# Kernel tuning notes

Hardware: AMD Instinct MI355X
Metric: run time of the kernel (lower is better)

Reference implementation:

```python
import jax, jax.numpy as jnp
import numpy as np

KERNEL = (3, 3, 3, 3)
PAD = (1, 1, 1, 1)
IN_CH = 8
OUT_CH = 8


def setup_inputs() -> dict:
    key = jax.random.key(0)
    k1, k2, k3 = jax.random.split(key, 3)
    x = jax.random.normal(k1, (2, IN_CH, 7, 7, 48, 48), dtype=jnp.float32)
    K = KERNEL[0] * KERNEL[1] * KERNEL[2] * KERNEL[3]
    conv = jax.random.normal(k2, (OUT_CH, K * IN_CH), dtype=jnp.float32) * 0.05
    bias = jax.random.normal(k3, (OUT_CH,), dtype=jnp.float32) * 0.05
    return {"x": x, "conv": conv, "bias": bias}


def reference(x, conv, bias):
    # x: (B, C, u, v, h, w); conv: (oc, k0*k1*k2*k3*C); bias: (oc,)
    B, C, u, v, h, w = x.shape
    oc = conv.shape[0]
    k0, k1, k2, k3 = KERNEL
    # torch unfold+permute orders the contraction axis as (k0,k1,k2,k3,C)
    W = conv.reshape(oc, k0, k1, k2, k3, C)
    xp = jnp.pad(x, ((0, 0), (0, 0),
                     (PAD[0], PAD[0]), (PAD[1], PAD[1]),
                     (PAD[2], PAD[2]), (PAD[3], PAD[3])))
    out = jnp.zeros((B, oc, u, v, h, w), dtype=x.dtype)
    # stride = 1 everywhere: accumulate over the 3^4 kernel offsets
    for i0 in range(k0):
        for i1 in range(k1):
            for i2 in range(k2):
                for i3 in range(k3):
                    xs = xp[:, :, i0:i0 + u, i1:i1 + v, i2:i2 + h, i3:i3 + w]
                    out = out + jnp.einsum('bcuvhw,oc->bouvhw', xs,
                                           W[:, i0, i1, i2, i3, :])
    out = out + bias[None, :, None, None, None, None]
    return out
```

## Files before the change

### kernel.cpp

```cpp
#include <hip/hip_runtime.h>


typedef __attribute__((ext_vector_type(8))) short short8;
typedef __attribute__((ext_vector_type(4))) float f32x4;
typedef __attribute__((ext_vector_type(2))) int   i32x2;

#define CSTRIDE (49 * 2304)
#define WP_OFF  3920000
#define WT_OFF  3940992

__device__ __forceinline__ unsigned short f2bf(float f) {
    union { float f; unsigned u; } v; v.f = f;
    unsigned u = v.u;
    return (unsigned short)((u + 0x7FFF + ((u >> 16) & 1)) >> 16);
}

__global__ __launch_bounds__(256)
void prep(const float* __restrict__ x, const float* __restrict__ conv,
          unsigned short* __restrict__ ws16) {
    int g = blockIdx.x * 256 + threadIdx.x;
    if (g < 245000) {
        unsigned short vals[8];
#pragma unroll
        for (int c = 0; c < 8; ++c) vals[c] = 0;
        int b  = g / 122500;
        int r  = g - b * 122500;
        int uv = r / 2500;
        int p  = r - uv * 2500;
        int hh = p / 50, ww = p - hh * 50;
        int h = hh - 1, w = ww - 1;
        if (((unsigned)h < 48u) && ((unsigned)w < 48u)) {
            const float* xb = x + ((size_t)b * 8 * 49 + uv) * 2304 + h * 48 + w;
#pragma unroll
            for (int c = 0; c < 8; ++c) vals[c] = f2bf(xb[(size_t)c * CSTRIDE]);
        }
        *(short8*)(ws16 + (size_t)g * 8) = *(const short8*)vals;
        return;
    }
    g -= 245000;
    if (g < 10496) {
        int tap = g >> 7;
        int r   = g & 127;
        int m   = r >> 3, j = r & 7;
        unsigned short v = 0;
        if (tap < 81 && m < 8) v = f2bf(conv[m * 648 + tap * 8 + j]);
        ws16[WP_OFF / 2 + g] = v;
        return;
    }
    g -= 10496;
    if (g < 8624) {
        int img  = g / 88, slot = g - img * 88;
        int b    = img / 49, uv = img - b * 49;
        int u    = uv / 7,   v  = uv - u * 7;
        int cu = 3 - (u == 0) - (u == 6);
        int cv = 3 - (v == 0) - (v == 6);
        int tab, wof;
        if (slot < cu * cv * 9) {
            int g9  = slot / 9, hw9 = slot - 9 * g9;
            int gi0 = g9 / cv,  gi1 = g9 - cv * gi0;
            int i0 = (u == 0) + gi0, i1 = (v == 0) + gi1;
            int uu = u + i0 - 1,     vv = v + i1 - 1;
            int i2 = hw9 / 3,        i3 = hw9 - 3 * i2;
            tab = (((b * 7 + uu) * 7 + vv) * 2500 + i2 * 50 + i3) * 16;
            wof = ((i0 * 3 + i1) * 9 + hw9) * 256;
        } else {
            tab = 0;
            wof = 81 * 256;
        }
        i32x2 e; e.x = tab; e.y = wof;
        *(i32x2*)((char*)ws16 + WT_OFF + (size_t)g * 8) = e;
    }
}

__global__ __launch_bounds__(128, 6)
void conv4d_mfma(const unsigned short* __restrict__ ws16,
                 const float* __restrict__ bias,
                 float* __restrict__ out) {
    const int img = blockIdx.y;
    const int b   = img / 49;
    const int uvr = img - b * 49;
    const int u   = uvr / 7;
    const int v   = uvr - u * 7;
    const int cu  = 3 - (u == 0) - (u == 6);
    const int cv  = 3 - (v == 0) - (v == 6);
    const int nchunk = (cu * cv * 9 + 3) >> 2;

    const int lane  = threadIdx.x & 63;
    const int wave  = threadIdx.x >> 6;
    const int n     = lane & 15;
    const int quad  = lane >> 4;
    const int sbase = blockIdx.x * 64 + wave * 32;

    int myoff0, myoff1;
    {
        int s0 = sbase + n;
        int h0 = s0 / 48, w0 = s0 - h0 * 48;
        myoff0 = (h0 * 50 + w0) * 16;
        int s1 = sbase + 16 + n;
        int h1 = s1 / 48, w1 = s1 - h1 * 48;
        myoff1 = (h1 * 50 + w1) * 16;
    }

    const char* base0 = (const char*)ws16;
    const char* wpb   = base0 + WP_OFF;
    const i32x2* tbl  = (const i32x2*)(base0 + WT_OFF) + img * 88;
    const int n16     = n * 16;

    i32x2 tw = tbl[quad];
    short8 wf  = *(const short8*)(wpb + tw.y + n16);
    short8 xf0 = *(const short8*)(base0 + tw.x + myoff0);
    short8 xf1 = *(const short8*)(base0 + tw.x + myoff1);

    f32x4 acc0 = (f32x4){0.f, 0.f, 0.f, 0.f};
    f32x4 acc1 = acc0;

    for (int c = 0; c < nchunk; ++c) {
        i32x2 twn = tbl[4 * (c + 1) + quad];
        short8 wfn  = *(const short8*)(wpb + twn.y + n16);
        short8 xf0n = *(const short8*)(base0 + twn.x + myoff0);
        short8 xf1n = *(const short8*)(base0 + twn.x + myoff1);
        acc0 = __builtin_amdgcn_mfma_f32_16x16x32_bf16(wf, xf0, acc0, 0, 0, 0);
        acc1 = __builtin_amdgcn_mfma_f32_16x16x32_bf16(wf, xf1, acc1, 0, 0, 0);
        wf = wfn; xf0 = xf0n; xf1 = xf1n;
    }

    if (quad < 2) {
        f32x4 bb = *(const f32x4*)(bias + quad * 4);
        float* ob = out + ((size_t)b * 8 * 49 + uvr) * 2304 + sbase + n;
#pragma unroll
        for (int r = 0; r < 4; ++r) {
            int o = quad * 4 + r;
            ob[(size_t)o * CSTRIDE]      = acc0[r] + bb[r];
            ob[(size_t)o * CSTRIDE + 16] = acc1[r] + bb[r];
        }
    }
}

extern "C" void kernel_launch(void* const* d_in, const int* in_sizes, int n_in,
                              void* d_out, int out_size, void* d_ws, size_t ws_size,
                              hipStream_t stream) {
    const float* x    = (const float*)d_in[0];
    const float* conv = (const float*)d_in[1];
    const float* bias = (const float*)d_in[2];
    float* out = (float*)d_out;
    unsigned short* ws16 = (unsigned short*)d_ws;

    prep<<<dim3((245000 + 10496 + 8624 + 255) / 256), dim3(256), 0, stream>>>(x, conv, ws16);
    conv4d_mfma<<<dim3(36, 98), dim3(128), 0, stream>>>(ws16, bias, out);
}
```

Before: 82.31 us.

## Pack tap table into single ints and fully unroll chunk loop with preloaded table

Each tap-table entry is packed into one 32-bit int holding the activation offset and weight-tap index, and a dedicated zero region replaces the padding entries. The conv kernel preloads all 21 table entries into registers up front and fully unrolls the MFMA chunk loop in three tiers (9, 14, 21 chunks) matching the possible boundary counts. This lets all gathers be issued early, removing the serial dependency on table loads in the software pipeline. The cost is more registers, so launch bounds are relaxed from 6 to 4 waves per SIMD, which may lower occupancy.

Result: faster. 78.59 us (-4.5%).

```diff
diff --git a/kernel.cpp b/kernel.cpp
--- a/kernel.cpp
+++ b/kernel.cpp
@@ -3,11 +3,11 @@
 
 typedef __attribute__((ext_vector_type(8))) short short8;
 typedef __attribute__((ext_vector_type(4))) float f32x4;
-typedef __attribute__((ext_vector_type(2))) int   i32x2;
 
 #define CSTRIDE (49 * 2304)
-#define WP_OFF  3920000
-#define WT_OFF  3940992
+#define ZS_OFF  3920000
+#define WP_OFF  3960000
+#define WT_OFF  3981504
 
 __device__ __forceinline__ unsigned short f2bf(float f) {
     union { float f; unsigned u; } v; v.f = f;
@@ -19,26 +19,28 @@
 void prep(const float* __restrict__ x, const float* __restrict__ conv,
           unsigned short* __restrict__ ws16) {
     int g = blockIdx.x * 256 + threadIdx.x;
-    if (g < 245000) {
+    if (g < 247500) {
         unsigned short vals[8];
 #pragma unroll
         for (int c = 0; c < 8; ++c) vals[c] = 0;
-        int b  = g / 122500;
-        int r  = g - b * 122500;
-        int uv = r / 2500;
-        int p  = r - uv * 2500;
-        int hh = p / 50, ww = p - hh * 50;
-        int h = hh - 1, w = ww - 1;
-        if (((unsigned)h < 48u) && ((unsigned)w < 48u)) {
-            const float* xb = x + ((size_t)b * 8 * 49 + uv) * 2304 + h * 48 + w;
+        if (g < 245000) {
+            int b  = g / 122500;
+            int r  = g - b * 122500;
+            int uv = r / 2500;
+            int p  = r - uv * 2500;
+            int hh = p / 50, ww = p - hh * 50;
+            int h = hh - 1, w = ww - 1;
+            if (((unsigned)h < 48u) && ((unsigned)w < 48u)) {
+                const float* xb = x + ((size_t)b * 8 * 49 + uv) * 2304 + h * 48 + w;
 #pragma unroll
-            for (int c = 0; c < 8; ++c) vals[c] = f2bf(xb[(size_t)c * CSTRIDE]);
+                for (int c = 0; c < 8; ++c) vals[c] = f2bf(xb[(size_t)c * CSTRIDE]);
+            }
         }
         *(short8*)(ws16 + (size_t)g * 8) = *(const short8*)vals;
         return;
     }
-    g -= 245000;
-    if (g < 10496) {
+    g -= 247500;
+    if (g < 10752) {
         int tap = g >> 7;
         int r   = g & 127;
         int m   = r >> 3, j = r & 7;
@@ -47,32 +49,31 @@
         ws16[WP_OFF / 2 + g] = v;
         return;
     }
-    g -= 10496;
+    g -= 10752;
     if (g < 8624) {
         int img  = g / 88, slot = g - img * 88;
         int b    = img / 49, uv = img - b * 49;
         int u    = uv / 7,   v  = uv - u * 7;
         int cu = 3 - (u == 0) - (u == 6);
         int cv = 3 - (v == 0) - (v == 6);
-        int tab, wof;
+        int entry;
         if (slot < cu * cv * 9) {
             int g9  = slot / 9, hw9 = slot - 9 * g9;
             int gi0 = g9 / cv,  gi1 = g9 - cv * gi0;
             int i0 = (u == 0) + gi0, i1 = (v == 0) + gi1;
             int uu = u + i0 - 1,     vv = v + i1 - 1;
             int i2 = hw9 / 3,        i3 = hw9 - 3 * i2;
-            tab = (((b * 7 + uu) * 7 + vv) * 2500 + i2 * 50 + i3) * 16;
-            wof = ((i0 * 3 + i1) * 9 + hw9) * 256;
+            int tab  = (((b * 7 + uu) * 7 + vv) * 2500 + i2 * 50 + i3) * 16;
+            int wtap = (i0 * 3 + i1) * 9 + hw9;
+            entry = tab | (wtap << 22);
         } else {
-            tab = 0;
-            wof = 81 * 256;
+            entry = ZS_OFF | (81 << 22);
         }
-        i32x2 e; e.x = tab; e.y = wof;
-        *(i32x2*)((char*)ws16 + WT_OFF + (size_t)g * 8) = e;
+        ((int*)((char*)ws16 + WT_OFF))[g] = entry;
     }
 }
 
-__global__ __launch_bounds__(128, 6)
+__global__ __launch_bounds__(128, 4)
 void conv4d_mfma(const unsigned short* __restrict__ ws16,
                  const float* __restrict__ bias,
                  float* __restrict__ out) {
@@ -103,26 +104,39 @@
 
     const char* base0 = (const char*)ws16;
     const char* wpb   = base0 + WP_OFF;
-    const i32x2* tbl  = (const i32x2*)(base0 + WT_OFF) + img * 88;
-    const int n16     = n * 16;
+    const int*  tblp  = (const int*)(base0 + WT_OFF) + img * 88;
+    const int   n16   = n * 16;
 
-    i32x2 tw = tbl[quad];
-    short8 wf  = *(const short8*)(wpb + tw.y + n16);
-    short8 xf0 = *(const short8*)(base0 + tw.x + myoff0);
-    short8 xf1 = *(const short8*)(base0 + tw.x + myoff1);
+    int t[21];
+#pragma unroll
+    for (int c = 0; c < 21; ++c) t[c] = tblp[4 * c + quad];
 
     f32x4 acc0 = (f32x4){0.f, 0.f, 0.f, 0.f};
     f32x4 acc1 = acc0;
 
-    for (int c = 0; c < nchunk; ++c) {
-        i32x2 twn = tbl[4 * (c + 1) + quad];
-        short8 wfn  = *(const short8*)(wpb + twn.y + n16);
-        short8 xf0n = *(const short8*)(base0 + twn.x + myoff0);
-        short8 xf1n = *(const short8*)(base0 + twn.x + myoff1);
-        acc0 = __builtin_amdgcn_mfma_f32_16x16x32_bf16(wf, xf0, acc0, 0, 0, 0);
-        acc1 = __builtin_amdgcn_mfma_f32_16x16x32_bf16(wf, xf1, acc1, 0, 0, 0);
-        wf = wfn; xf0 = xf0n; xf1 = xf1n;
+#define CHUNK(c)                                                              \
+    {                                                                         \
+        int e   = t[c];                                                       \
+        int tab = e & 0x3FFFFF;                                               \
+        int wof = (e >> 22) << 8;                                             \
+        short8 wf  = *(const short8*)(wpb + wof + n16);                       \
+        short8 xf0 = *(const short8*)(base0 + tab + myoff0);                  \
+        short8 xf1 = *(const short8*)(base0 + tab + myoff1);                  \
+        acc0 = __builtin_amdgcn_mfma_f32_16x16x32_bf16(wf, xf0, acc0, 0, 0, 0); \
+        acc1 = __builtin_amdgcn_mfma_f32_16x16x32_bf16(wf, xf1, acc1, 0, 0, 0); \
     }
+
+#pragma unroll
+    for (int c = 0; c < 9; ++c) CHUNK(c);
+    if (nchunk > 9) {
+#pragma unroll
+        for (int c = 9; c < 14; ++c) CHUNK(c);
+        if (nchunk > 14) {
+#pragma unroll
+            for (int c = 14; c < 21; ++c) CHUNK(c);
+        }
+    }
+#undef CHUNK
 
     if (quad < 2) {
         f32x4 bb = *(const f32x4*)(bias + quad * 4);
@@ -145,6 +159,6 @@
     float* out = (float*)d_out;
     unsigned short* ws16 = (unsigned short*)d_ws;
 
-    prep<<<dim3((245000 + 10496 + 8624 + 255) / 256), dim3(256), 0, stream>>>(x, conv, ws16);
+    prep<<<dim3((247500 + 10752 + 8624 + 255) / 256), dim3(256), 0, stream>>>(x, conv, ws16);
     conv4d_mfma<<<dim3(36, 98), dim3(128), 0, stream>>>(ws16, bias, out);
 }
```
